# Kernel tuning notes

Hardware: AMD Instinct MI355X
Metric: run time of the kernel (lower is better)

## Reference

```python
import jax, jax.numpy as jnp
import numpy as np

TEMPERATURE = 4.0

def setup_inputs() -> dict:
    key = jax.random.key(0)
    k1, k2 = jax.random.split(key)
    query = jax.random.normal(k1, (128, 128, 256), dtype=jnp.float32)      # (B, D, Q)
    context = jax.random.normal(k2, (128, 128, 32, 32), dtype=jnp.float32)  # (B, D, H, W)
    return {"query": query, "context": context}

def reference(query, context):
    B, D, Q = query.shape
    H, W = context.shape[2], context.shape[3]
    L = H * W  # context_length
    context_flat = context.reshape(B, D, L)                    # (B, D, L)
    # scores[b, l, q] = sum_d context[b, d, l] * query[b, d, q]
    scores = jnp.einsum('bdl,bdq->blq', context_flat, query)   # (B, L, Q)
    # first softmax: over query dim (context -> query)
    attn_q = jax.nn.softmax(scores, axis=-1)                   # (B, L, Q)
    # second softmax: over context dim with temperature (query -> context)
    attn_c = jax.nn.softmax(attn_q.transpose(0, 2, 1) * TEMPERATURE, axis=-1)  # (B, Q, L)
    # weighted_context[b, d, q] = sum_l context[b, d, l] * attn_c[b, q, l]
    weighted_context = jnp.einsum('bdl,bql->bdq', context_flat, attn_c)  # (B, D, Q)
    attention_map = attn_c.reshape(B, Q, H, W)
    return (weighted_context, attention_map)
```

## Files before the change

### kernel.cpp

```cpp
#include <hip/hip_runtime.h>
#include <math.h>

#define B_ 128
#define D_ 128
#define Q_ 256
#define L_ 1024
#define BLK ((size_t)B_ * L_)

typedef __attribute__((ext_vector_type(8))) short s16x8;
typedef __attribute__((ext_vector_type(4))) float f32x4;

__device__ __forceinline__ unsigned short f2bf(float x) {
  unsigned u = __float_as_uint(x);
  u += 0x7FFF + ((u >> 16) & 1);
  return (unsigned short)(u >> 16);
}
__device__ __forceinline__ float bf2f(unsigned short h) {
  return __uint_as_float(((unsigned)h) << 16);
}
__device__ __forceinline__ uint2 pack4bf(float4 v) {
  uint2 r;
  r.x = ((unsigned)f2bf(v.y) << 16) | (unsigned)f2bf(v.x);
  r.y = ((unsigned)f2bf(v.w) << 16) | (unsigned)f2bf(v.z);
  return r;
}

__global__ __launch_bounds__(256) void k1_scores(
    const float* __restrict__ query, const float* __restrict__ ctx,
    float* __restrict__ S, float* __restrict__ pm, float* __restrict__ ps) {
  __shared__ float Af[32][129];
  __shared__ float Bf[32][129];
  __shared__ float sm[2][128], ss[2][128];

  const int b = blockIdx.z, qt = blockIdx.y;
  const int q0 = qt * 128, l0 = blockIdx.x * 128;
  const int tid = threadIdx.x;
  const int w = tid >> 6, lane = tid & 63, quad = lane >> 4, l15 = lane & 15;
  const int wq = w >> 1, wl = w & 1;

  const float* Qb = query + (size_t)b * D_ * Q_;
  const float* Cb = ctx + (size_t)b * D_ * L_;

  f32x4 acc[4][4];
#pragma unroll
  for (int mi = 0; mi < 4; mi++)
#pragma unroll
    for (int ni = 0; ni < 4; ni++) acc[mi][ni] = (f32x4){0.f, 0.f, 0.f, 0.f};

  const int cc = (tid & 31) * 4;
  const int kr = tid >> 5;

  for (int k0 = 0; k0 < D_; k0 += 32) {
    if (k0) __syncthreads();
#pragma unroll
    for (int h = 0; h < 4; h++) {
      const int k = kr + h * 8;
      *(float4*)&Af[k][cc] =
          *(const float4*)(Qb + (size_t)(k0 + k) * Q_ + q0 + cc);
      *(float4*)&Bf[k][cc] =
          *(const float4*)(Cb + (size_t)(k0 + k) * L_ + l0 + cc);
    }
    __syncthreads();

    s16x8 ah[4], al[4], bh[4], bl[4];
#pragma unroll
    for (int mi = 0; mi < 4; mi++) {
      const int row = wq * 64 + mi * 16 + l15;
#pragma unroll
      for (int j = 0; j < 8; j++) {
        float x = Af[quad * 8 + j][row];
        unsigned short h1 = f2bf(x);
        ah[mi][j] = (short)h1;
        al[mi][j] = (short)f2bf(x - bf2f(h1));
      }
    }
#pragma unroll
    for (int ni = 0; ni < 4; ni++) {
      const int row = wl * 64 + ni * 16 + l15;
#pragma unroll
      for (int j = 0; j < 8; j++) {
        float x = Bf[quad * 8 + j][row];
        unsigned short h1 = f2bf(x);
        bh[ni][j] = (short)h1;
        bl[ni][j] = (short)f2bf(x - bf2f(h1));
      }
    }
#pragma unroll
    for (int mi = 0; mi < 4; mi++)
#pragma unroll
      for (int ni = 0; ni < 4; ni++) {
        acc[mi][ni] = __builtin_amdgcn_mfma_f32_16x16x32_bf16(
            ah[mi], bh[ni], acc[mi][ni], 0, 0, 0);
        acc[mi][ni] = __builtin_amdgcn_mfma_f32_16x16x32_bf16(
            ah[mi], bl[ni], acc[mi][ni], 0, 0, 0);
        acc[mi][ni] = __builtin_amdgcn_mfma_f32_16x16x32_bf16(
            al[mi], bh[ni], acc[mi][ni], 0, 0, 0);
      }
  }

  float* Sb = S + ((size_t)b * Q_ + q0) * L_ + l0;
#pragma unroll
  for (int mi = 0; mi < 4; mi++)
#pragma unroll
    for (int ni = 0; ni < 4; ni++)
#pragma unroll
      for (int r = 0; r < 4; r++)
        Sb[(size_t)(wq * 64 + mi * 16 + quad * 4 + r) * L_ + wl * 64 +
           ni * 16 + l15] = acc[mi][ni][r];

#pragma unroll
  for (int ni = 0; ni < 4; ni++) {
    float m = -1e30f;
#pragma unroll
    for (int mi = 0; mi < 4; mi++)
#pragma unroll
      for (int r = 0; r < 4; r++) m = fmaxf(m, acc[mi][ni][r]);
    m = fmaxf(m, __shfl_xor(m, 16));
    m = fmaxf(m, __shfl_xor(m, 32));
    float s = 0.f;
#pragma unroll
    for (int mi = 0; mi < 4; mi++)
#pragma unroll
      for (int r = 0; r < 4; r++) s += __expf(acc[mi][ni][r] - m);
    s += __shfl_xor(s, 16);
    s += __shfl_xor(s, 32);
    if (quad == 0) {
      sm[wq][wl * 64 + ni * 16 + l15] = m;
      ss[wq][wl * 64 + ni * 16 + l15] = s;
    }
  }
  __syncthreads();
  if (tid < 128) {
    float m0 = sm[0][tid], m1 = sm[1][tid];
    float M = fmaxf(m0, m1);
    float Sv = ss[0][tid] * __expf(m0 - M) + ss[1][tid] * __expf(m1 - M);
    pm[(size_t)qt * BLK + (size_t)b * L_ + l0 + tid] = M;
    ps[(size_t)qt * BLK + (size_t)b * L_ + l0 + tid] = Sv;
  }
}

__global__ __launch_bounds__(256) void k2_combine(
    const float* __restrict__ pm, const float* __restrict__ ps,
    float* __restrict__ fm, float* __restrict__ fs) {
  const size_t i = (size_t)blockIdx.x * 256 + threadIdx.x;
  float m0 = pm[i], m1 = pm[BLK + i];
  float M = fmaxf(m0, m1);
  float s = ps[i] * __expf(m0 - M) + ps[BLK + i] * __expf(m1 - M);
  fm[i] = M;
  fs[i] = s;
}

__global__ __launch_bounds__(256) void k3_softmax2(
    float* __restrict__ S, const float* __restrict__ fm,
    const float* __restrict__ fs) {
  const int q = blockIdx.x;
  const int b = blockIdx.y;
  const int t = threadIdx.x;
  const int l = t * 4;
  float* row = S + ((size_t)b * Q_ + q) * L_;
  float4 sv = *(const float4*)(row + l);
  float4 mx = *(const float4*)(fm + (size_t)b * L_ + l);
  float4 smv = *(const float4*)(fs + (size_t)b * L_ + l);
  float t0 = __expf(4.f * (__expf(sv.x - mx.x) / smv.x));
  float t1 = __expf(4.f * (__expf(sv.y - mx.y) / smv.y));
  float t2 = __expf(4.f * (__expf(sv.z - mx.z) / smv.z));
  float t3 = __expf(4.f * (__expf(sv.w - mx.w) / smv.w));
  float tot = t0 + t1 + t2 + t3;
#pragma unroll
  for (int off = 32; off > 0; off >>= 1) tot += __shfl_xor(tot, off);
  __shared__ float red[4];
  if ((t & 63) == 0) red[t >> 6] = tot;
  __syncthreads();
  const float inv = 1.f / (red[0] + red[1] + red[2] + red[3]);
  float4 o = make_float4(t0 * inv, t1 * inv, t2 * inv, t3 * inv);
  *(float4*)(row + l) = o;
}

__global__ __launch_bounds__(256) void k4_weighted(
    const float* __restrict__ ctx, const float* __restrict__ attn,
    float* __restrict__ W) {
  __shared__ unsigned short As[128][32];
  __shared__ unsigned short Bs[64][32];
  const int b = blockIdx.y, q0 = blockIdx.x * 64;
  const int tid = threadIdx.x;
  const int w = tid >> 6, lane = tid & 63, quad = lane >> 4, l15 = lane & 15;
  const int wd = (w >> 1) * 64, wn = (w & 1) * 32;

  const float* Cb = ctx + (size_t)b * D_ * L_;
  const float* Ab = attn + ((size_t)b * Q_ + q0) * L_;

  f32x4 acc[4][2];
#pragma unroll
  for (int mi = 0; mi < 4; mi++)
#pragma unroll
    for (int ni = 0; ni < 2; ni++) acc[mi][ni] = (f32x4){0.f, 0.f, 0.f, 0.f};

  const int lc = (tid & 7) * 4;
  const int rr = tid >> 3;

  for (int l0 = 0; l0 < L_; l0 += 32) {
    if (l0) __syncthreads();
#pragma unroll
    for (int h = 0; h < 4; h++) {
      const int d = rr + h * 32;
      float4 cv = *(const float4*)(Cb + (size_t)d * L_ + l0 + lc);
      *(uint2*)&As[d][lc] = pack4bf(cv);
    }
#pragma unroll
    for (int h = 0; h < 2; h++) {
      const int q = rr + h * 32;
      float4 av = *(const float4*)(Ab + (size_t)q * L_ + l0 + lc);
      *(uint2*)&Bs[q][lc] = pack4bf(av);
    }
    __syncthreads();

    s16x8 af[4], bq[2];
#pragma unroll
    for (int mi = 0; mi < 4; mi++)
      af[mi] = *(const s16x8*)&As[wd + mi * 16 + l15][quad * 8];
#pragma unroll
    for (int ni = 0; ni < 2; ni++)
      bq[ni] = *(const s16x8*)&Bs[wn + ni * 16 + l15][quad * 8];
#pragma unroll
    for (int mi = 0; mi < 4; mi++)
#pragma unroll
      for (int ni = 0; ni < 2; ni++)
        acc[mi][ni] = __builtin_amdgcn_mfma_f32_16x16x32_bf16(
            af[mi], bq[ni], acc[mi][ni], 0, 0, 0);
  }

  float* Wb = W + (size_t)b * D_ * Q_;
#pragma unroll
  for (int mi = 0; mi < 4; mi++)
#pragma unroll
    for (int ni = 0; ni < 2; ni++)
#pragma unroll
      for (int r = 0; r < 4; r++)
        Wb[(size_t)(wd + mi * 16 + quad * 4 + r) * Q_ + q0 + wn + ni * 16 +
           l15] = acc[mi][ni][r];
}

extern "C" void kernel_launch(void* const* d_in, const int* in_sizes, int n_in,
                              void* d_out, int out_size, void* d_ws,
                              size_t ws_size, hipStream_t stream) {
  const float* query = (const float*)d_in[0];
  const float* ctx = (const float*)d_in[1];
  float* W = (float*)d_out;
  float* S = (float*)d_out + (size_t)B_ * D_ * Q_;
  float* pm = W;
  float* ps = W + 2 * BLK;
  float* fm = W + 4 * BLK;
  float* fs = W + 5 * BLK;

  k1_scores<<<dim3(L_ / 128, Q_ / 128, B_), 256, 0, stream>>>(query, ctx, S,
                                                              pm, ps);
  k2_combine<<<dim3((unsigned)(BLK / 256)), 256, 0, stream>>>(pm, ps, fm, fs);
  k3_softmax2<<<dim3(Q_, B_), 256, 0, stream>>>(S, fm, fs);
  k4_weighted<<<dim3(Q_ / 64, B_), 256, 0, stream>>>(ctx, S, W);
}
```

Measured before the change: 331.9 us.

## Fuse first softmax into score GEMM and second softmax into weighted GEMM

The score kernel now covers all 256 queries per 64-column L tile, so the query-axis softmax finishes inside the block. It writes normalized attn_q directly and emits partial column sums of exp(4*a) for the second softmax. A small kernel reduces those partials to inverse denominators, and the weighted-context GEMM applies exp(4a)*invd while loading, writing the final attention map in place. This removes a full read-modify-write pass over the 128MB attention tensor plus the combine kernel. In exchange the GEMM loads global memory directly without shared-memory staging, which may uncoalesce the strided query/context reads.

```diff
diff --git a/kernel.cpp b/kernel.cpp
--- a/kernel.cpp
+++ b/kernel.cpp
@@ -5,7 +5,6 @@
 #define D_ 128
 #define Q_ 256
 #define L_ 1024
-#define BLK ((size_t)B_ * L_)
 
 typedef __attribute__((ext_vector_type(8))) short s16x8;
 typedef __attribute__((ext_vector_type(4))) float f32x4;
@@ -24,22 +23,27 @@
   r.y = ((unsigned)f2bf(v.w) << 16) | (unsigned)f2bf(v.z);
   return r;
 }
-
-__global__ __launch_bounds__(256) void k1_scores(
+__device__ __forceinline__ void split8(const float* x, s16x8& hi, s16x8& lo) {
+#pragma unroll
+  for (int j = 0; j < 8; j++) {
+    unsigned short h = f2bf(x[j]);
+    hi[j] = (short)h;
+    lo[j] = (short)f2bf(x[j] - bf2f(h));
+  }
+}
+
+__global__ __launch_bounds__(256, 2) void k1_attnq(
     const float* __restrict__ query, const float* __restrict__ ctx,
-    float* __restrict__ S, float* __restrict__ pm, float* __restrict__ ps) {
-  __shared__ float Af[32][129];
-  __shared__ float Bf[32][129];
-  __shared__ float sm[2][128], ss[2][128];
-
-  const int b = blockIdx.z, qt = blockIdx.y;
-  const int q0 = qt * 128, l0 = blockIdx.x * 128;
+    float* __restrict__ attq, float* __restrict__ pd) {
+  __shared__ float sm[4][64], ss[4][64], fm[64], fs[64];
+  const int lt = blockIdx.x, b = blockIdx.y;
+  const int l0 = lt * 64;
   const int tid = threadIdx.x;
-  const int w = tid >> 6, lane = tid & 63, quad = lane >> 4, l15 = lane & 15;
-  const int wq = w >> 1, wl = w & 1;
+  const int wq = tid >> 6;
+  const int lane = tid & 63, quad = lane >> 4, l15 = lane & 15;
 
   const float* Qb = query + (size_t)b * D_ * Q_;
-  const float* Cb = ctx + (size_t)b * D_ * L_;
+  const float* Cb = ctx + (size_t)b * D_ * L_ + l0;
 
   f32x4 acc[4][4];
 #pragma unroll
@@ -47,43 +51,25 @@
 #pragma unroll
     for (int ni = 0; ni < 4; ni++) acc[mi][ni] = (f32x4){0.f, 0.f, 0.f, 0.f};
 
-  const int cc = (tid & 31) * 4;
-  const int kr = tid >> 5;
-
+#pragma unroll 2
   for (int k0 = 0; k0 < D_; k0 += 32) {
-    if (k0) __syncthreads();
-#pragma unroll
-    for (int h = 0; h < 4; h++) {
-      const int k = kr + h * 8;
-      *(float4*)&Af[k][cc] =
-          *(const float4*)(Qb + (size_t)(k0 + k) * Q_ + q0 + cc);
-      *(float4*)&Bf[k][cc] =
-          *(const float4*)(Cb + (size_t)(k0 + k) * L_ + l0 + cc);
-    }
-    __syncthreads();
-
+    const int kq = k0 + quad * 8;
     s16x8 ah[4], al[4], bh[4], bl[4];
 #pragma unroll
     for (int mi = 0; mi < 4; mi++) {
-      const int row = wq * 64 + mi * 16 + l15;
-#pragma unroll
-      for (int j = 0; j < 8; j++) {
-        float x = Af[quad * 8 + j][row];
-        unsigned short h1 = f2bf(x);
-        ah[mi][j] = (short)h1;
-        al[mi][j] = (short)f2bf(x - bf2f(h1));
-      }
+      const float* p = Qb + (size_t)kq * Q_ + wq * 64 + mi * 16 + l15;
+      float x[8];
+#pragma unroll
+      for (int j = 0; j < 8; j++) x[j] = p[(size_t)j * Q_];
+      split8(x, ah[mi], al[mi]);
     }
 #pragma unroll
     for (int ni = 0; ni < 4; ni++) {
-      const int row = wl * 64 + ni * 16 + l15;
-#pragma unroll
-      for (int j = 0; j < 8; j++) {
-        float x = Bf[quad * 8 + j][row];
-        unsigned short h1 = f2bf(x);
-        bh[ni][j] = (short)h1;
-        bl[ni][j] = (short)f2bf(x - bf2f(h1));
-      }
+      const float* p = Cb + (size_t)kq * L_ + ni * 16 + l15;
+      float x[8];
+#pragma unroll
+      for (int j = 0; j < 8; j++) x[j] = p[(size_t)j * L_];
+      split8(x, bh[ni], bl[ni]);
     }
 #pragma unroll
     for (int mi = 0; mi < 4; mi++)
@@ -97,16 +83,6 @@
             al[mi], bh[ni], acc[mi][ni], 0, 0, 0);
       }
   }
-
-  float* Sb = S + ((size_t)b * Q_ + q0) * L_ + l0;
-#pragma unroll
-  for (int mi = 0; mi < 4; mi++)
-#pragma unroll
-    for (int ni = 0; ni < 4; ni++)
-#pragma unroll
-      for (int r = 0; r < 4; r++)
-        Sb[(size_t)(wq * 64 + mi * 16 + quad * 4 + r) * L_ + wl * 64 +
-           ni * 16 + l15] = acc[mi][ni][r];
 
 #pragma unroll
   for (int ni = 0; ni < 4; ni++) {
@@ -125,60 +101,78 @@
     s += __shfl_xor(s, 16);
     s += __shfl_xor(s, 32);
     if (quad == 0) {
-      sm[wq][wl * 64 + ni * 16 + l15] = m;
-      ss[wq][wl * 64 + ni * 16 + l15] = s;
+      sm[wq][ni * 16 + l15] = m;
+      ss[wq][ni * 16 + l15] = s;
     }
   }
   __syncthreads();
-  if (tid < 128) {
-    float m0 = sm[0][tid], m1 = sm[1][tid];
-    float M = fmaxf(m0, m1);
-    float Sv = ss[0][tid] * __expf(m0 - M) + ss[1][tid] * __expf(m1 - M);
-    pm[(size_t)qt * BLK + (size_t)b * L_ + l0 + tid] = M;
-    ps[(size_t)qt * BLK + (size_t)b * L_ + l0 + tid] = Sv;
-  }
-}
-
-__global__ __launch_bounds__(256) void k2_combine(
-    const float* __restrict__ pm, const float* __restrict__ ps,
-    float* __restrict__ fm, float* __restrict__ fs) {
-  const size_t i = (size_t)blockIdx.x * 256 + threadIdx.x;
-  float m0 = pm[i], m1 = pm[BLK + i];
-  float M = fmaxf(m0, m1);
-  float s = ps[i] * __expf(m0 - M) + ps[BLK + i] * __expf(m1 - M);
-  fm[i] = M;
-  fs[i] = s;
-}
-
-__global__ __launch_bounds__(256) void k3_softmax2(
-    float* __restrict__ S, const float* __restrict__ fm,
-    const float* __restrict__ fs) {
-  const int q = blockIdx.x;
-  const int b = blockIdx.y;
-  const int t = threadIdx.x;
-  const int l = t * 4;
-  float* row = S + ((size_t)b * Q_ + q) * L_;
-  float4 sv = *(const float4*)(row + l);
-  float4 mx = *(const float4*)(fm + (size_t)b * L_ + l);
-  float4 smv = *(const float4*)(fs + (size_t)b * L_ + l);
-  float t0 = __expf(4.f * (__expf(sv.x - mx.x) / smv.x));
-  float t1 = __expf(4.f * (__expf(sv.y - mx.y) / smv.y));
-  float t2 = __expf(4.f * (__expf(sv.z - mx.z) / smv.z));
-  float t3 = __expf(4.f * (__expf(sv.w - mx.w) / smv.w));
-  float tot = t0 + t1 + t2 + t3;
-#pragma unroll
-  for (int off = 32; off > 0; off >>= 1) tot += __shfl_xor(tot, off);
-  __shared__ float red[4];
-  if ((t & 63) == 0) red[t >> 6] = tot;
+  if (tid < 64) {
+    float m0 = sm[0][tid], m1 = sm[1][tid], m2 = sm[2][tid], m3 = sm[3][tid];
+    float M = fmaxf(fmaxf(m0, m1), fmaxf(m2, m3));
+    float S = ss[0][tid] * __expf(m0 - M) + ss[1][tid] * __expf(m1 - M) +
+              ss[2][tid] * __expf(m2 - M) + ss[3][tid] * __expf(m3 - M);
+    fm[tid] = M;
+    fs[tid] = 1.f / S;
+  }
   __syncthreads();
-  const float inv = 1.f / (red[0] + red[1] + red[2] + red[3]);
-  float4 o = make_float4(t0 * inv, t1 * inv, t2 * inv, t3 * inv);
-  *(float4*)(row + l) = o;
+
+  float fmv[4], fiv[4];
+#pragma unroll
+  for (int ni = 0; ni < 4; ni++) {
+    fmv[ni] = fm[ni * 16 + l15];
+    fiv[ni] = fs[ni * 16 + l15];
+  }
+  float* Ab = attq + ((size_t)b * Q_ + wq * 64) * L_ + l0;
+  float dsum[4][4];
+#pragma unroll
+  for (int mi = 0; mi < 4; mi++)
+#pragma unroll
+    for (int r = 0; r < 4; r++) dsum[mi][r] = 0.f;
+#pragma unroll
+  for (int mi = 0; mi < 4; mi++)
+#pragma unroll
+    for (int r = 0; r < 4; r++) {
+      const int q = mi * 16 + quad * 4 + r;
+#pragma unroll
+      for (int ni = 0; ni < 4; ni++) {
+        float a = __expf(acc[mi][ni][r] - fmv[ni]) * fiv[ni];
+        Ab[(size_t)q * L_ + ni * 16 + l15] = a;
+        dsum[mi][r] += __expf(4.f * a);
+      }
+    }
+#pragma unroll
+  for (int mi = 0; mi < 4; mi++)
+#pragma unroll
+    for (int r = 0; r < 4; r++) {
+      float v = dsum[mi][r];
+      v += __shfl_xor(v, 1);
+      v += __shfl_xor(v, 2);
+      v += __shfl_xor(v, 4);
+      v += __shfl_xor(v, 8);
+      dsum[mi][r] = v;
+    }
+  if (l15 == 0) {
+#pragma unroll
+    for (int mi = 0; mi < 4; mi++)
+#pragma unroll
+      for (int r = 0; r < 4; r++)
+        pd[(size_t)lt * (B_ * Q_) + b * Q_ + wq * 64 + mi * 16 + quad * 4 +
+           r] = dsum[mi][r];
+  }
+}
+
+__global__ __launch_bounds__(256) void k2_invd(const float* __restrict__ pd,
+                                               float* __restrict__ invd) {
+  const int i = blockIdx.x * 256 + threadIdx.x;
+  float s = 0.f;
+#pragma unroll
+  for (int t = 0; t < 16; t++) s += pd[(size_t)t * (B_ * Q_) + i];
+  invd[i] = 1.f / s;
 }
 
 __global__ __launch_bounds__(256) void k4_weighted(
-    const float* __restrict__ ctx, const float* __restrict__ attn,
-    float* __restrict__ W) {
+    const float* __restrict__ ctx, float* __restrict__ attn,
+    const float* __restrict__ invd, float* __restrict__ W) {
   __shared__ unsigned short As[128][32];
   __shared__ unsigned short Bs[64][32];
   const int b = blockIdx.y, q0 = blockIdx.x * 64;
@@ -187,16 +181,18 @@
   const int wd = (w >> 1) * 64, wn = (w & 1) * 32;
 
   const float* Cb = ctx + (size_t)b * D_ * L_;
-  const float* Ab = attn + ((size_t)b * Q_ + q0) * L_;
-
-  f32x4 acc[4][2];
-#pragma unroll
-  for (int mi = 0; mi < 4; mi++)
-#pragma unroll
-    for (int ni = 0; ni < 2; ni++) acc[mi][ni] = (f32x4){0.f, 0.f, 0.f, 0.f};
+  float* Ab = attn + ((size_t)b * Q_ + q0) * L_;
 
   const int lc = (tid & 7) * 4;
   const int rr = tid >> 3;
+  const float id0 = invd[b * Q_ + q0 + rr];
+  const float id1 = invd[b * Q_ + q0 + rr + 32];
+
+  f32x4 acc[4][2];
+#pragma unroll
+  for (int mi = 0; mi < 4; mi++)
+#pragma unroll
+    for (int ni = 0; ni < 2; ni++) acc[mi][ni] = (f32x4){0.f, 0.f, 0.f, 0.f};
 
   for (int l0 = 0; l0 < L_; l0 += 32) {
     if (l0) __syncthreads();
@@ -209,8 +205,16 @@
 #pragma unroll
     for (int h = 0; h < 2; h++) {
       const int q = rr + h * 32;
-      float4 av = *(const float4*)(Ab + (size_t)q * L_ + l0 + lc);
-      *(uint2*)&Bs[q][lc] = pack4bf(av);
+      float* p = Ab + (size_t)q * L_ + l0 + lc;
+      float4 a = *(const float4*)p;
+      const float idv = h ? id1 : id0;
+      float4 t;
+      t.x = __expf(4.f * a.x) * idv;
+      t.y = __expf(4.f * a.y) * idv;
+      t.z = __expf(4.f * a.z) * idv;
+      t.w = __expf(4.f * a.w) * idv;
+      *(float4*)p = t;
+      *(uint2*)&Bs[q][lc] = pack4bf(t);
     }
     __syncthreads();
 
@@ -246,15 +250,13 @@
   const float* query = (const float*)d_in[0];
   const float* ctx = (const float*)d_in[1];
   float* W = (float*)d_out;
-  float* S = (float*)d_out + (size_t)B_ * D_ * Q_;
-  float* pm = W;
-  float* ps = W + 2 * BLK;
-  float* fm = W + 4 * BLK;
-  float* fs = W + 5 * BLK;
-
-  k1_scores<<<dim3(L_ / 128, Q_ / 128, B_), 256, 0, stream>>>(query, ctx, S,
-                                                              pm, ps);
-  k2_combine<<<dim3((unsigned)(BLK / 256)), 256, 0, stream>>>(pm, ps, fm, fs);
-  k3_softmax2<<<dim3(Q_, B_), 256, 0, stream>>>(S, fm, fs);
-  k4_weighted<<<dim3(Q_ / 64, B_), 256, 0, stream>>>(ctx, S, W);
-}
+  float* attn = (float*)d_out + (size_t)B_ * D_ * Q_;
+
+  const size_t need = (size_t)17 * B_ * Q_ * sizeof(float);
+  float* pd = (ws_size >= need && d_ws) ? (float*)d_ws : W;
+  float* invd = pd + (size_t)16 * B_ * Q_;
+
+  k1_attnq<<<dim3(L_ / 64, B_), 256, 0, stream>>>(query, ctx, attn, pd);
+  k2_invd<<<dim3(B_ * Q_ / 256), 256, 0, stream>>>(pd, invd);
+  k4_weighted<<<dim3(Q_ / 64, B_), 256, 0, stream>>>(ctx, attn, invd, W);
+}
```

Measured after the change: 316.8 us. 4.5% less time.
